# Optimization experiments

Hardware: AMD Instinct MI355X
Metric: run time of the kernel (lower is better)

## Reference

```python
import jax, jax.numpy as jnp
import numpy as np

N, IN_SIZE, OUT_SIZE = 8192, 256, 64


def setup_inputs() -> dict:
    key = jax.random.key(0)
    kx, kw, kb = jax.random.split(key, 3)
    x = jax.random.normal(kx, (N, IN_SIZE), dtype=jnp.float32)
    # Per-feature Linear(1, out_size): weight w[i] (shape [out_size]) and bias b[i].
    # torch.nn.Linear(1, out_size) init: U(-1, 1) since fan_in = 1.
    W = jax.random.uniform(kw, (IN_SIZE, OUT_SIZE), minval=-1.0, maxval=1.0, dtype=jnp.float32)
    b = jax.random.uniform(kb, (IN_SIZE, OUT_SIZE), minval=-1.0, maxval=1.0, dtype=jnp.float32)
    return {"x": x, "W": W, "b": b}


def reference(x, W, b):
    # x: [N, F]; W, b: [F, D]
    # layer_i(x[:, i:i+1]) = x[:, i, None] * W[i] + b[i]  -> stacked [N, D, F] in torch,
    # here [N, F, D]; mean over feature axis is identical either way.
    out = x[:, :, None] * W[None, :, :] + b[None, :, :]  # [N, F, D]
    out = jnp.nan_to_num(out)
    return out.mean(axis=1)  # [N, D]
```

## Files before the change

kernel.cpp:

```cpp
#include <hip/hip_runtime.h>
#include <stdint.h>

#define NROWS 8192
#define FDIM  256
#define DDIM  64

typedef __attribute__((ext_vector_type(8))) short short8;
typedef __attribute__((ext_vector_type(4))) float floatx4;

__device__ inline unsigned int pack2_bf16(float a, float b) {
    unsigned int ua = __float_as_uint(a);
    unsigned int ub = __float_as_uint(b);
    ua += 0x7fffu + ((ua >> 16) & 1u);
    ub += 0x7fffu + ((ub >> 16) & 1u);
    return (ua >> 16) | (ub & 0xffff0000u);
}

__global__ __launch_bounds__(128)
void nanembed_mfma(const float* __restrict__ x,
                   const float* __restrict__ W,
                   const float* __restrict__ b,
                   float* __restrict__ out)
{
    __shared__ __align__(16) unsigned int bfrag_lds[2048 * 4];
    __shared__ float4 bias_part[8][16];

    const int tid  = threadIdx.x;
    const int lane = tid & 63;
    const int w    = tid >> 6;
    const int q    = lane >> 4;
    const int n    = lane & 15;
    const int r0   = blockIdx.x * 32;

    const int row = r0 + w * 16 + n;
    const float4* xp = reinterpret_cast<const float4*>(x + (size_t)row * FDIM + q * 8);
    float4 xv[16];
    #pragma unroll
    for (int ks = 0; ks < 8; ++ks) {
        xv[2 * ks]     = xp[ks * 8];
        xv[2 * ks + 1] = xp[ks * 8 + 1];
    }

    #pragma unroll
    for (int i = 0; i < 16; ++i) {
        int f  = tid + i * 128;
        int ks = f >> 8;
        int nt = (f >> 6) & 3;
        int fl = f & 63;
        int fq = fl >> 4;
        int c  = nt * 16 + (fl & 15);
        const float* wp = W + (size_t)(ks * 32 + fq * 8) * DDIM + c;
        union { short8 s; unsigned int u[4]; } fr;
        fr.u[0] = pack2_bf16(wp[0 * DDIM], wp[1 * DDIM]);
        fr.u[1] = pack2_bf16(wp[2 * DDIM], wp[3 * DDIM]);
        fr.u[2] = pack2_bf16(wp[4 * DDIM], wp[5 * DDIM]);
        fr.u[3] = pack2_bf16(wp[6 * DDIM], wp[7 * DDIM]);
        reinterpret_cast<short8*>(bfrag_lds)[f] = fr.s;
    }

    {
        const int c4 = tid & 15;
        const int h  = tid >> 4;
        const float4* bp = reinterpret_cast<const float4*>(b) + c4;
        float4 s = make_float4(0.f, 0.f, 0.f, 0.f);
        #pragma unroll 8
        for (int f = h * 32; f < h * 32 + 32; ++f) {
            float4 v = bp[(size_t)f * 16];
            s.x += v.x; s.y += v.y; s.z += v.z; s.w += v.w;
        }
        bias_part[h][c4] = s;
    }

    __syncthreads();

    floatx4 acc[4] = {{0.f, 0.f, 0.f, 0.f}, {0.f, 0.f, 0.f, 0.f},
                      {0.f, 0.f, 0.f, 0.f}, {0.f, 0.f, 0.f, 0.f}};
    #pragma unroll
    for (int ks = 0; ks < 8; ++ks) {
        union { short8 s; unsigned int u[4]; } fa;
        float4 v0 = xv[2 * ks], v1 = xv[2 * ks + 1];
        fa.u[0] = pack2_bf16(v0.x, v0.y);
        fa.u[1] = pack2_bf16(v0.z, v0.w);
        fa.u[2] = pack2_bf16(v1.x, v1.y);
        fa.u[3] = pack2_bf16(v1.z, v1.w);
        #pragma unroll
        for (int nt = 0; nt < 4; ++nt) {
            short8 fb = reinterpret_cast<const short8*>(bfrag_lds)[ks * 256 + nt * 64 + lane];
            acc[nt] = __builtin_amdgcn_mfma_f32_16x16x32_bf16(fa.s, fb, acc[nt], 0, 0, 0);
        }
    }

    #pragma unroll
    for (int nt = 0; nt < 4; ++nt) {
        const int c = nt * 16 + n;
        float bs = 0.f;
        #pragma unroll
        for (int h = 0; h < 8; ++h)
            bs += reinterpret_cast<const float*>(&bias_part[h][0])[c];
        #pragma unroll
        for (int reg = 0; reg < 4; ++reg) {
            const int r = r0 + w * 16 + q * 4 + reg;
            out[(size_t)r * DDIM + c] = (acc[nt][reg] + bs) * (1.0f / 256.0f);
        }
    }
}

extern "C" void kernel_launch(void* const* d_in, const int* in_sizes, int n_in,
                              void* d_out, int out_size, void* d_ws, size_t ws_size,
                              hipStream_t stream) {
    const float* x = (const float*)d_in[0];
    const float* W = (const float*)d_in[1];
    const float* b = (const float*)d_in[2];
    float* out = (float*)d_out;

    nanembed_mfma<<<dim3(NROWS / 32), 128, 0, stream>>>(x, W, b, out);
}
```

Before: 65.27 us.

## Precompute bf16 W fragments and bias sums once, split K across waves

W is now converted to bf16 MFMA fragments and b is reduced over features once, in a small prep kernel that writes both to workspace. Before, every block redid this work for itself. The main kernel loads the fragments straight into registers and splits the feature (K) dimension across two waves with an LDS reduction, running 512 blocks of 16 rows instead of 256 blocks of 32. This removes redundant per-block W packing and bias summation, at the cost of a second kernel launch and a dependency through global memory.

```diff
diff --git a/kernel.cpp b/kernel.cpp
--- a/kernel.cpp
+++ b/kernel.cpp
@@ -16,67 +16,77 @@
     return (ua >> 16) | (ub & 0xffff0000u);
 }
 
-__global__ __launch_bounds__(128)
-void nanembed_mfma(const float* __restrict__ x,
-                   const float* __restrict__ W,
-                   const float* __restrict__ b,
-                   float* __restrict__ out)
+__global__ __launch_bounds__(256)
+void nanembed_prep(const float* __restrict__ W, const float* __restrict__ b,
+                   unsigned int* __restrict__ ws)
 {
-    __shared__ __align__(16) unsigned int bfrag_lds[2048 * 4];
-    __shared__ float4 bias_part[8][16];
-
-    const int tid  = threadIdx.x;
-    const int lane = tid & 63;
-    const int w    = tid >> 6;
-    const int q    = lane >> 4;
-    const int n    = lane & 15;
-    const int r0   = blockIdx.x * 32;
-
-    const int row = r0 + w * 16 + n;
-    const float4* xp = reinterpret_cast<const float4*>(x + (size_t)row * FDIM + q * 8);
-    float4 xv[16];
-    #pragma unroll
-    for (int ks = 0; ks < 8; ++ks) {
-        xv[2 * ks]     = xp[ks * 8];
-        xv[2 * ks + 1] = xp[ks * 8 + 1];
-    }
-
-    #pragma unroll
-    for (int i = 0; i < 16; ++i) {
-        int f  = tid + i * 128;
-        int ks = f >> 8;
-        int nt = (f >> 6) & 3;
-        int fl = f & 63;
-        int fq = fl >> 4;
-        int c  = nt * 16 + (fl & 15);
-        const float* wp = W + (size_t)(ks * 32 + fq * 8) * DDIM + c;
+    const int t   = threadIdx.x;
+    const int blk = blockIdx.x;
+    if (blk < 8) {
+        const int f  = blk * 256 + t;
+        const int ks = f >> 8;
+        const int fl = f & 63;
+        const int c  = ((f >> 6) & 3) * 16 + (fl & 15);
+        const float* wp = W + (size_t)(ks * 32 + (fl >> 4) * 8) * DDIM + c;
         union { short8 s; unsigned int u[4]; } fr;
         fr.u[0] = pack2_bf16(wp[0 * DDIM], wp[1 * DDIM]);
         fr.u[1] = pack2_bf16(wp[2 * DDIM], wp[3 * DDIM]);
         fr.u[2] = pack2_bf16(wp[4 * DDIM], wp[5 * DDIM]);
         fr.u[3] = pack2_bf16(wp[6 * DDIM], wp[7 * DDIM]);
-        reinterpret_cast<short8*>(bfrag_lds)[f] = fr.s;
+        reinterpret_cast<short8*>(ws)[f] = fr.s;
+    } else {
+        __shared__ float part[4][64];
+        const int c     = t & 63;
+        const int seg   = t >> 6;
+        const int fbase = (blk - 8) * 64 + seg * 16;
+        float s = 0.f;
+        #pragma unroll
+        for (int i = 0; i < 16; ++i)
+            s += b[(size_t)(fbase + i) * DDIM + c];
+        part[seg][c] = s;
+        __syncthreads();
+        if (t < 64) {
+            reinterpret_cast<float*>(ws)[8192 + (blk - 8) * 64 + t] =
+                part[0][t] + part[1][t] + part[2][t] + part[3][t];
+        }
+    }
+}
+
+__global__ __launch_bounds__(128)
+void nanembed_main(const float* __restrict__ x,
+                   const unsigned int* __restrict__ ws,
+                   float* __restrict__ out)
+{
+    __shared__ floatx4 red[4][64];
+
+    const int tid  = threadIdx.x;
+    const int lane = tid & 63;
+    const int wk   = tid >> 6;
+    const int q    = lane >> 4;
+    const int n    = lane & 15;
+    const int r0   = blockIdx.x * 16;
+
+    const float4* xp = reinterpret_cast<const float4*>(x + (size_t)(r0 + n) * FDIM)
+                       + (wk * 32 + q * 2);
+    float4 xv[8];
+    #pragma unroll
+    for (int ks = 0; ks < 4; ++ks) {
+        xv[2 * ks]     = xp[ks * 8];
+        xv[2 * ks + 1] = xp[ks * 8 + 1];
     }
 
-    {
-        const int c4 = tid & 15;
-        const int h  = tid >> 4;
-        const float4* bp = reinterpret_cast<const float4*>(b) + c4;
-        float4 s = make_float4(0.f, 0.f, 0.f, 0.f);
-        #pragma unroll 8
-        for (int f = h * 32; f < h * 32 + 32; ++f) {
-            float4 v = bp[(size_t)f * 16];
-            s.x += v.x; s.y += v.y; s.z += v.z; s.w += v.w;
-        }
-        bias_part[h][c4] = s;
-    }
-
-    __syncthreads();
+    const short8* wf = reinterpret_cast<const short8*>(ws);
+    short8 bf[4][4];
+    #pragma unroll
+    for (int ks = 0; ks < 4; ++ks)
+        #pragma unroll
+        for (int nt = 0; nt < 4; ++nt)
+            bf[ks][nt] = wf[(wk * 4 + ks) * 256 + nt * 64 + lane];
 
     floatx4 acc[4] = {{0.f, 0.f, 0.f, 0.f}, {0.f, 0.f, 0.f, 0.f},
                       {0.f, 0.f, 0.f, 0.f}, {0.f, 0.f, 0.f, 0.f}};
     #pragma unroll
-    for (int ks = 0; ks < 8; ++ks) {
+    for (int ks = 0; ks < 4; ++ks) {
         union { short8 s; unsigned int u[4]; } fa;
         float4 v0 = xv[2 * ks], v1 = xv[2 * ks + 1];
         fa.u[0] = pack2_bf16(v0.x, v0.y);
@@ -84,23 +94,29 @@
         fa.u[2] = pack2_bf16(v1.x, v1.y);
         fa.u[3] = pack2_bf16(v1.z, v1.w);
         #pragma unroll
-        for (int nt = 0; nt < 4; ++nt) {
-            short8 fb = reinterpret_cast<const short8*>(bfrag_lds)[ks * 256 + nt * 64 + lane];
-            acc[nt] = __builtin_amdgcn_mfma_f32_16x16x32_bf16(fa.s, fb, acc[nt], 0, 0, 0);
-        }
+        for (int nt = 0; nt < 4; ++nt)
+            acc[nt] = __builtin_amdgcn_mfma_f32_16x16x32_bf16(fa.s, bf[ks][nt], acc[nt], 0, 0, 0);
     }
 
-    #pragma unroll
-    for (int nt = 0; nt < 4; ++nt) {
-        const int c = nt * 16 + n;
-        float bs = 0.f;
+    if (wk == 1) {
         #pragma unroll
-        for (int h = 0; h < 8; ++h)
-            bs += reinterpret_cast<const float*>(&bias_part[h][0])[c];
+        for (int nt = 0; nt < 4; ++nt)
+            red[nt][lane] = acc[nt];
+    }
+    __syncthreads();
+
+    if (wk == 0) {
+        const float* pc = reinterpret_cast<const float*>(ws) + 8192;
         #pragma unroll
-        for (int reg = 0; reg < 4; ++reg) {
-            const int r = r0 + w * 16 + q * 4 + reg;
-            out[(size_t)r * DDIM + c] = (acc[nt][reg] + bs) * (1.0f / 256.0f);
+        for (int nt = 0; nt < 4; ++nt) {
+            floatx4 o = red[nt][lane];
+            const int c = nt * 16 + n;
+            const float bs = pc[c] + pc[64 + c] + pc[128 + c] + pc[192 + c];
+            #pragma unroll
+            for (int reg = 0; reg < 4; ++reg) {
+                const int r = r0 + q * 4 + reg;
+                out[(size_t)r * DDIM + c] = (acc[nt][reg] + o[reg] + bs) * (1.0f / 256.0f);
+            }
         }
     }
 }
@@ -112,6 +128,8 @@
     const float* W = (const float*)d_in[1];
     const float* b = (const float*)d_in[2];
     float* out = (float*)d_out;
+    unsigned int* ws = (unsigned int*)d_ws;
 
-    nanembed_mfma<<<dim3(NROWS / 32), 128, 0, stream>>>(x, W, b, out);
+    nanembed_prep<<<dim3(12), 256, 0, stream>>>(W, b, ws);
+    nanembed_main<<<dim3(512), 128, 0, stream>>>(x, ws, out);
 }
```

After: 63.34 us. 1.03x faster.

## Split K across four waves with LDS reduction, 16 rows per block

Applied to the files above, without the earlier changes.

Work is now split along the feature (K) dimension: each of four waves handles a quarter of the 256 features for 16 rows. The partial MFMA accumulators are then reduced through LDS, reusing the fragment buffer. Blocks now cover 16 rows with 256 threads, which doubles the grid to 512 blocks and shrinks per-thread register use, aiming for more parallelism and occupancy. The cost is that every block still converts the full W to bf16 and sums the full bias, so that redundant per-block work doubles, and two extra barriers plus an LDS reduction are added.

```diff
diff --git a/kernel.cpp b/kernel.cpp
--- a/kernel.cpp
+++ b/kernel.cpp
@@ -16,46 +16,44 @@
     return (ua >> 16) | (ub & 0xffff0000u);
 }
 
-__global__ __launch_bounds__(128)
-void nanembed_mfma(const float* __restrict__ x,
-                   const float* __restrict__ W,
-                   const float* __restrict__ b,
-                   float* __restrict__ out)
+__global__ __launch_bounds__(256, 2)
+void nanembed_fused(const float* __restrict__ x,
+                    const float* __restrict__ W,
+                    const float* __restrict__ b,
+                    float* __restrict__ out)
 {
-    __shared__ __align__(16) unsigned int bfrag_lds[2048 * 4];
-    __shared__ float4 bias_part[8][16];
+    __shared__ __align__(16) unsigned int frag_lds[2048 * 4];
+    __shared__ float4 bias_part[16][16];
 
     const int tid  = threadIdx.x;
     const int lane = tid & 63;
-    const int w    = tid >> 6;
+    const int wk   = tid >> 6;
     const int q    = lane >> 4;
     const int n    = lane & 15;
-    const int r0   = blockIdx.x * 32;
+    const int r0   = blockIdx.x * 16;
 
-    const int row = r0 + w * 16 + n;
-    const float4* xp = reinterpret_cast<const float4*>(x + (size_t)row * FDIM + q * 8);
-    float4 xv[16];
+    const float4* xp = reinterpret_cast<const float4*>(x)
+                       + (size_t)(r0 + n) * 64 + wk * 16 + q * 2;
+    float4 xv[4];
     #pragma unroll
-    for (int ks = 0; ks < 8; ++ks) {
+    for (int ks = 0; ks < 2; ++ks) {
         xv[2 * ks]     = xp[ks * 8];
         xv[2 * ks + 1] = xp[ks * 8 + 1];
     }
 
     #pragma unroll
-    for (int i = 0; i < 16; ++i) {
-        int f  = tid + i * 128;
-        int ks = f >> 8;
-        int nt = (f >> 6) & 3;
-        int fl = f & 63;
-        int fq = fl >> 4;
-        int c  = nt * 16 + (fl & 15);
-        const float* wp = W + (size_t)(ks * 32 + fq * 8) * DDIM + c;
+    for (int i = 0; i < 8; ++i) {
+        const int f  = tid + i * 256;
+        const int ks = f >> 8;
+        const int fl = f & 63;
+        const int c  = ((f >> 6) & 3) * 16 + (fl & 15);
+        const float* wp = W + (size_t)(ks * 32 + (fl >> 4) * 8) * DDIM + c;
         union { short8 s; unsigned int u[4]; } fr;
         fr.u[0] = pack2_bf16(wp[0 * DDIM], wp[1 * DDIM]);
         fr.u[1] = pack2_bf16(wp[2 * DDIM], wp[3 * DDIM]);
         fr.u[2] = pack2_bf16(wp[4 * DDIM], wp[5 * DDIM]);
         fr.u[3] = pack2_bf16(wp[6 * DDIM], wp[7 * DDIM]);
-        reinterpret_cast<short8*>(bfrag_lds)[f] = fr.s;
+        reinterpret_cast<short8*>(frag_lds)[f] = fr.s;
     }
 
     {
@@ -63,8 +61,8 @@
         const int h  = tid >> 4;
         const float4* bp = reinterpret_cast<const float4*>(b) + c4;
         float4 s = make_float4(0.f, 0.f, 0.f, 0.f);
-        #pragma unroll 8
-        for (int f = h * 32; f < h * 32 + 32; ++f) {
+        #pragma unroll
+        for (int f = h * 16; f < h * 16 + 16; ++f) {
             float4 v = bp[(size_t)f * 16];
             s.x += v.x; s.y += v.y; s.z += v.z; s.w += v.w;
         }
@@ -76,7 +74,7 @@
     floatx4 acc[4] = {{0.f, 0.f, 0.f, 0.f}, {0.f, 0.f, 0.f, 0.f},
                       {0.f, 0.f, 0.f, 0.f}, {0.f, 0.f, 0.f, 0.f}};
     #pragma unroll
-    for (int ks = 0; ks < 8; ++ks) {
+    for (int ks = 0; ks < 2; ++ks) {
         union { short8 s; unsigned int u[4]; } fa;
         float4 v0 = xv[2 * ks], v1 = xv[2 * ks + 1];
         fa.u[0] = pack2_bf16(v0.x, v0.y);
@@ -85,22 +83,39 @@
         fa.u[3] = pack2_bf16(v1.z, v1.w);
         #pragma unroll
         for (int nt = 0; nt < 4; ++nt) {
-            short8 fb = reinterpret_cast<const short8*>(bfrag_lds)[ks * 256 + nt * 64 + lane];
+            short8 fb = reinterpret_cast<const short8*>(frag_lds)
+                            [(wk * 2 + ks) * 256 + nt * 64 + lane];
             acc[nt] = __builtin_amdgcn_mfma_f32_16x16x32_bf16(fa.s, fb, acc[nt], 0, 0, 0);
         }
     }
 
-    #pragma unroll
-    for (int nt = 0; nt < 4; ++nt) {
-        const int c = nt * 16 + n;
-        float bs = 0.f;
+    __syncthreads();
+    floatx4* red = reinterpret_cast<floatx4*>(frag_lds);
+    if (wk != 0) {
         #pragma unroll
-        for (int h = 0; h < 8; ++h)
-            bs += reinterpret_cast<const float*>(&bias_part[h][0])[c];
+        for (int nt = 0; nt < 4; ++nt)
+            red[((wk - 1) * 4 + nt) * 64 + lane] = acc[nt];
+    }
+    __syncthreads();
+
+    if (wk == 0) {
+        const float* pb = reinterpret_cast<const float*>(bias_part);
         #pragma unroll
-        for (int reg = 0; reg < 4; ++reg) {
-            const int r = r0 + w * 16 + q * 4 + reg;
-            out[(size_t)r * DDIM + c] = (acc[nt][reg] + bs) * (1.0f / 256.0f);
+        for (int nt = 0; nt < 4; ++nt) {
+            floatx4 o0 = red[(0 * 4 + nt) * 64 + lane];
+            floatx4 o1 = red[(1 * 4 + nt) * 64 + lane];
+            floatx4 o2 = red[(2 * 4 + nt) * 64 + lane];
+            const int c = nt * 16 + n;
+            float bs = 0.f;
+            #pragma unroll
+            for (int h = 0; h < 16; ++h)
+                bs += pb[h * 64 + c];
+            #pragma unroll
+            for (int reg = 0; reg < 4; ++reg) {
+                const int r = r0 + q * 4 + reg;
+                out[(size_t)r * DDIM + c] =
+                    (acc[nt][reg] + o0[reg] + o1[reg] + o2[reg] + bs) * (1.0f / 256.0f);
+            }
         }
     }
 }
@@ -113,5 +128,5 @@
     const float* b = (const float*)d_in[2];
     float* out = (float*)d_out;
 
-    nanembed_mfma<<<dim3(NROWS / 32), 128, 0, stream>>>(x, W, b, out);
+    nanembed_fused<<<dim3(NROWS / 16), 256, 0, stream>>>(x, W, b, out);
 }
```

After: 64.69 us. About the same (-0.9%).
